# Kernel optimization log

Hardware: AMD Instinct MI355X
Metric: run time of the kernel (lower is better)

## Reference

```python
import jax, jax.numpy as jnp
import numpy as np

B, N, SK, D, H = 4, 1024, 1024, 1024, 16
HD = D // H  # head_dim = 64


def _ln(x, w, b):
    # torch LayerNorm: biased variance, eps=1e-6
    m = x.mean(-1, keepdims=True)
    v = x.var(-1, keepdims=True)
    return (x - m) * jax.lax.rsqrt(v + 1e-6) * w + b


def setup_inputs() -> dict:
    key = jax.random.key(0)
    ks = jax.random.split(key, 16)
    def w(k, shape, s=0.02):
        return jax.random.normal(k, shape, jnp.float32) * s
    return dict(
        x=jax.random.normal(ks[0], (B, N, D), jnp.float32),
        k=jax.random.normal(ks[1], (N, H, SK, HD), jnp.float32),
        v=jax.random.normal(ks[2], (N, H, SK, HD), jnp.float32),
        qkv_w=w(ks[3], (D, 3 * D)), qkv_b=w(ks[4], (3 * D,)),
        sa_proj_w=w(ks[5], (D, D)), sa_proj_b=w(ks[6], (D,)),
        q_w=w(ks[7], (D, D)), q_b=w(ks[8], (D,)),
        ed_proj_w=w(ks[9], (D, D)), ed_proj_b=w(ks[10], (D,)),
        fc1_w=w(ks[11], (D, 4 * D)), fc1_b=w(ks[12], (4 * D,)),
        fc2_w=w(ks[13], (4 * D, D)), fc2_b=w(ks[14], (D,)),
        ln1_w=jnp.ones((D,)), ln1_b=jnp.zeros((D,)),
        ln2_w=jnp.ones((D,)), ln2_b=jnp.zeros((D,)),
        ln3_w=jnp.ones((D,)), ln3_b=jnp.zeros((D,)),
    )


def reference(x, k, v, qkv_w, qkv_b, sa_proj_w, sa_proj_b, q_w, q_b,
              ed_proj_w, ed_proj_b, fc1_w, fc1_b, fc2_w, fc2_b,
              ln1_w, ln1_b, ln2_w, ln2_b, ln3_w, ln3_b):
    scale = HD ** -0.5
    # ---- SelfAttention (faithful to the original, unusual einsums) ----
    qkv = (x @ qkv_w + qkv_b).reshape(B, N, 3, H, HD).transpose(2, 1, 3, 0, 4)
    q_s, k_s, v_s = qkv[0], qkv[1], qkv[2]  # each [N, H, B, HD]
    # no shared contraction index between k and q -> outer product of reductions
    dp = jnp.einsum('kabc,qdef->qabe', k_s, q_s) * scale  # [N, H, B, B]
    sc = jax.nn.softmax(dp, axis=-1)  # attn_p = 0.0 -> dropout is identity
    wa = jnp.einsum('qabc,kdef->bqaf', sc, v_s).reshape(B, N, D)
    sa = wa @ sa_proj_w + sa_proj_b
    h1 = _ln(sa + x, ln1_w, ln1_b)
    # ---- EncoderDecoderAttention ----
    qc = (h1 @ q_w + q_b).reshape(B, N, H, HD).transpose(1, 2, 0, 3)  # [N, H, B, HD]
    dp2 = jnp.einsum('abkd,abqd->abqk', k, qc) * scale  # [N, H, B, SK]
    sc2 = jax.nn.softmax(dp2, axis=-1)
    wa2 = jnp.einsum('abts,abse->tabe', sc2, v).reshape(B, N, D)
    ca = wa2 @ ed_proj_w + ed_proj_b
    h2 = _ln(ca + x, ln2_w, ln2_b)  # residual uses x (as in source)
    # ---- MLP (exact GELU, p=0 dropout) ----
    z = jax.nn.gelu(h2 @ fc1_w + fc1_b, approximate=False) @ fc2_w + fc2_b
    return _ln(z + h2, ln3_w, ln3_b)
```

## Files before the change

### kernel.cpp

```cpp
#include <hip/hip_runtime.h>
#include <hip/hip_bf16.h>
#include <math.h>

typedef __attribute__((ext_vector_type(8))) short bf16x8;
typedef __attribute__((ext_vector_type(4))) float f32x4;

__device__ __forceinline__ void gll16(const void* g, const void* l) {
  __builtin_amdgcn_global_load_lds((__attribute__((address_space(1))) void*)g,
                                   (__attribute__((address_space(3))) void*)l, 16, 0, 0);
}

__device__ __forceinline__ unsigned short bf16bits(float f) {
  __hip_bfloat16 h = __float2bfloat16(f);
  return *reinterpret_cast<unsigned short*>(&h);
}

__global__ __launch_bounds__(256) void k_transpose4(
    const float* __restrict__ W0, __hip_bfloat16* __restrict__ T0,
    const float* __restrict__ W1, __hip_bfloat16* __restrict__ T1,
    const float* __restrict__ W2, __hip_bfloat16* __restrict__ T2,
    const float* __restrict__ W3, __hip_bfloat16* __restrict__ T3)
{
  __shared__ float t[32][33];
  int b = blockIdx.x;
  const float* W; __hip_bfloat16* T; int R, C, bx, by;
  if (b < 1024)      { W = W0; T = T0; R = 1024; C = 1024; bx = b & 31;  by = b >> 5; }
  else if (b < 2048) { b -= 1024; W = W1; T = T1; R = 1024; C = 1024; bx = b & 31;  by = b >> 5; }
  else if (b < 6144) { b -= 2048; W = W2; T = T2; R = 1024; C = 4096; bx = b & 127; by = b >> 7; }
  else               { b -= 6144; W = W3; T = T3; R = 4096; C = 1024; bx = b & 31;  by = b >> 5; }
  const int c0 = bx << 5, r0 = by << 5;
  const int tx = threadIdx.x & 31, ty = threadIdx.x >> 5;
#pragma unroll
  for (int i = 0; i < 32; i += 8)
    t[ty + i][tx] = W[(size_t)(r0 + ty + i) * C + c0 + tx];
  __syncthreads();
#pragma unroll
  for (int i = 0; i < 32; i += 8)
    T[(size_t)(c0 + ty + i) * R + r0 + tx] = __float2bfloat16(t[tx][ty + i]);
}

__global__ __launch_bounds__(256) void k_colsum_part(const float* __restrict__ x, float* __restrict__ part) {
  const int d = blockIdx.x * 256 + threadIdx.x;
  const int r0 = blockIdx.y * 128;
  float acc = 0.f;
  for (int r = 0; r < 128; ++r) acc += x[(size_t)(r0 + r) * 1024 + d];
  part[blockIdx.y * 1024 + d] = acc;
}

__global__ __launch_bounds__(256) void k_matvec_t(const float* __restrict__ part,
                                                  const float* __restrict__ qkv_w,
                                                  float* __restrict__ tmpt) {
  __shared__ float xs[1024];
  __shared__ float red[8][32];
#pragma unroll
  for (int jj = 0; jj < 4; ++jj) {
    const int d = threadIdx.x + (jj << 8);
    float a = 0.f;
    for (int y = 0; y < 32; ++y) a += part[y * 1024 + d];
    xs[d] = a;
  }
  __syncthreads();
  const int j = blockIdx.x * 32 + (threadIdx.x & 31);
  const int rg = threadIdx.x >> 5;
  float acc = 0.f;
  for (int r = rg; r < 1024; r += 8)
    acc += xs[r] * qkv_w[(size_t)r * 3072 + 2048 + j];
  red[rg][threadIdx.x & 31] = acc;
  __syncthreads();
  if (threadIdx.x < 32) {
    float s = 0.f;
    for (int gq = 0; gq < 8; ++gq) s += red[gq][threadIdx.x];
    tmpt[blockIdx.x * 32 + threadIdx.x] = s;
  }
}

__global__ __launch_bounds__(256) void k_matvec_sa(const float* __restrict__ tmpt,
                                                   const float* __restrict__ qkv_b,
                                                   const float* __restrict__ saw,
                                                   const float* __restrict__ sab,
                                                   float* __restrict__ sarow) {
  __shared__ float vs[64];
  __shared__ float red[8][32];
  if (threadIdx.x < 64) {
    float a = 0.f;
    for (int h = 0; h < 16; ++h)
      a += tmpt[h * 64 + threadIdx.x] + 4096.0f * qkv_b[2048 + h * 64 + threadIdx.x];
    vs[threadIdx.x] = a;
  }
  __syncthreads();
  const int j = blockIdx.x * 32 + (threadIdx.x & 31);
  const int rg = threadIdx.x >> 5;
  float acc = 0.f;
  for (int r = rg; r < 1024; r += 8)
    acc += vs[r & 63] * saw[(size_t)r * 1024 + j];
  red[rg][threadIdx.x & 31] = acc;
  __syncthreads();
  if (threadIdx.x < 32) {
    float s = 0.f;
    for (int gq = 0; gq < 8; ++gq) s += red[gq][threadIdx.x];
    sarow[blockIdx.x * 32 + threadIdx.x] = s + sab[blockIdx.x * 32 + threadIdx.x];
  }
}

__global__ __launch_bounds__(256) void k_ln(
    const float* __restrict__ a, const float* __restrict__ b, const float* __restrict__ c,
    const float* __restrict__ rowadd, const float* __restrict__ w,
    const float* __restrict__ bias, float* __restrict__ outF,
    __hip_bfloat16* __restrict__ outB)
{
  const size_t base = (size_t)blockIdx.x * 1024;
  const int d4 = threadIdx.x << 2;
  float4 t = *(const float4*)(a + base + d4);
  if (b) { const float4 u = *(const float4*)(b + base + d4);
           t.x += u.x; t.y += u.y; t.z += u.z; t.w += u.w; }
  if (c) { const float4 u = *(const float4*)(c + base + d4);
           t.x += u.x; t.y += u.y; t.z += u.z; t.w += u.w; }
  if (rowadd) { const float4 u = *(const float4*)(rowadd + d4);
                t.x += u.x; t.y += u.y; t.z += u.z; t.w += u.w; }
  float s1 = t.x + t.y + t.z + t.w;
  float s2 = t.x * t.x + t.y * t.y + t.z * t.z + t.w * t.w;
#pragma unroll
  for (int o = 32; o; o >>= 1) { s1 += __shfl_xor(s1, o); s2 += __shfl_xor(s2, o); }
  __shared__ float r1[4], r2[4];
  const int wv = threadIdx.x >> 6;
  if ((threadIdx.x & 63) == 0) { r1[wv] = s1; r2[wv] = s2; }
  __syncthreads();
  s1 = r1[0] + r1[1] + r1[2] + r1[3];
  s2 = r2[0] + r2[1] + r2[2] + r2[3];
  const float mean = s1 * (1.0f / 1024.0f);
  const float var = s2 * (1.0f / 1024.0f) - mean * mean;
  const float inv = rsqrtf(var + 1e-6f);
  const float4 w4 = *(const float4*)(w + d4);
  const float4 b4 = *(const float4*)(bias + d4);
  const float y0 = (t.x - mean) * inv * w4.x + b4.x;
  const float y1 = (t.y - mean) * inv * w4.y + b4.y;
  const float y2 = (t.z - mean) * inv * w4.z + b4.z;
  const float y3 = (t.w - mean) * inv * w4.w + b4.w;
  if (outF) *(float4*)(outF + base + d4) = make_float4(y0, y1, y2, y3);
  if (outB) {
    ushort4 u4; u4.x = bf16bits(y0); u4.y = bf16bits(y1); u4.z = bf16bits(y2); u4.w = bf16bits(y3);
    *(ushort4*)(outB + base + d4) = u4;
  }
}

template<int GELU, int OUTBF>
__global__ __launch_bounds__(256) void k_gemm_bt(
    const __hip_bfloat16* __restrict__ A, const __hip_bfloat16* __restrict__ BT,
    const float* __restrict__ bias, float* __restrict__ outF, float* __restrict__ outF2,
    __hip_bfloat16* __restrict__ outB, int M, int N, int K)
{
  __shared__ __align__(16) __hip_bfloat16 As[128 * 32];
  __shared__ __align__(16) __hip_bfloat16 Bs[128 * 32];
  const int tid = threadIdx.x;
  const int wave = tid >> 6, lane = tid & 63;
  const int m0 = blockIdx.y << 7, n0 = blockIdx.x << 7;
  const int kl = K / gridDim.z;
  const int ks = blockIdx.z * kl;
  float* outP = blockIdx.z ? outF2 : outF;
  const bool doBias = (blockIdx.z == 0);
  const int wr = wave >> 1, wc = wave & 1;
  const int fr = lane & 15, fq = lane >> 4;
  f32x4 acc[4][4] = {};
  const int srow = (lane >> 2);
  const int scol = (lane & 3) * 8;
  for (int k0 = ks; k0 < ks + kl; k0 += 32) {
#pragma unroll
    for (int i = 0; i < 2; ++i) {
      const int chunk = wave * 2 + i;
      const int row = (chunk << 4) + srow;
      gll16(A + (size_t)(m0 + row) * K + k0 + scol, As + (chunk << 9));
      gll16(BT + (size_t)(n0 + row) * K + k0 + scol, Bs + (chunk << 9));
    }
    __syncthreads();
    bf16x8 af[4], bfr[4];
#pragma unroll
    for (int m = 0; m < 4; ++m)
      af[m] = *(const bf16x8*)(As + ((wr << 6) + (m << 4) + fr) * 32 + (fq << 3));
#pragma unroll
    for (int nn = 0; nn < 4; ++nn)
      bfr[nn] = *(const bf16x8*)(Bs + ((wc << 6) + (nn << 4) + fr) * 32 + (fq << 3));
#pragma unroll
    for (int m = 0; m < 4; ++m)
#pragma unroll
      for (int nn = 0; nn < 4; ++nn)
        acc[m][nn] = __builtin_amdgcn_mfma_f32_16x16x32_bf16(af[m], bfr[nn], acc[m][nn], 0, 0, 0);
    __syncthreads();
  }
#pragma unroll
  for (int m = 0; m < 4; ++m) {
#pragma unroll
    for (int nn = 0; nn < 4; ++nn) {
      const int col = n0 + (wc << 6) + (nn << 4) + fr;
      const float bv = doBias ? bias[col] : 0.f;
#pragma unroll
      for (int j = 0; j < 4; ++j) {
        const int row = m0 + (wr << 6) + (m << 4) + (fq << 2) + j;
        float vv = acc[m][nn][j] + bv;
        if (GELU) vv = 0.5f * vv * (1.0f + erff(vv * 0.70710678118654752f));
        if (OUTBF) outB[(size_t)row * N + col] = __float2bfloat16(vv);
        else       outP[(size_t)row * N + col] = vv;
      }
    }
  }
}

__global__ __launch_bounds__(256) void k_attn(
    const float* __restrict__ kk, const float* __restrict__ vvg,
    const float* __restrict__ qc1, const float* __restrict__ qc2,
    __hip_bfloat16* __restrict__ wa2b)
{
  __shared__ __align__(16) float tile[2][32 * 64];
  __shared__ float p[4 * 1024];
  __shared__ __align__(16) float ql[4 * 64];
  const int tid = threadIdx.x;
  const int wave = tid >> 6, lane = tid & 63;
  const int n = blockIdx.x >> 4, h = blockIdx.x & 15;
  const size_t kvbase = (size_t)(n * 16 + h) * (1024 * 64);

  {
    const size_t qidx = ((size_t)wave * 1024 + n) * 1024 + h * 64 + lane;
    ql[tid] = (qc1[qidx] + qc2[qidx]) * 0.125f;
  }
  const float* qrow = ql + wave * 64;

  auto STAGE = [&](const float* __restrict__ src, int bi, int s0) {
#pragma unroll
    for (int i = 0; i < 2; ++i) {
      const int chunk = (wave << 1) + i;
      const int rl = (chunk << 2) + (lane >> 4);
      const int slot = (lane & 15) ^ (rl & 15);
      gll16(src + kvbase + (size_t)(s0 + rl) * 64 + (slot << 2), tile[bi] + (chunk << 8));
    }
  };

  STAGE(kk, 0, 0);
  __syncthreads();

  const int sl = lane & 31;
  const int dbase = (lane >> 5) << 3;
  const int sxx = sl & 15;
  for (int t = 0; t < 32; ++t) {
    if (t < 31) STAGE(kk, (t + 1) & 1, (t + 1) << 5);
    else        STAGE(vvg, 0, 0);
    const float* tl = tile[t & 1];
    float a = 0.f;
#pragma unroll
    for (int j = 0; j < 8; ++j) {
      const int c = dbase + j;
      const float4 kv = *(const float4*)(tl + sl * 64 + ((c ^ sxx) << 2));
      const float4 qa = *(const float4*)(qrow + (c << 2));
      a += kv.x * qa.x + kv.y * qa.y + kv.z * qa.z + kv.w * qa.w;
    }
    a += __shfl_xor(a, 32);
    if (lane < 32) p[(wave << 10) + (t << 5) + sl] = a;
    __syncthreads();
  }

  float mx = -1e30f;
#pragma unroll
  for (int j = 0; j < 16; ++j) mx = fmaxf(mx, p[(wave << 10) + (j << 6) + lane]);
#pragma unroll
  for (int o = 32; o; o >>= 1) mx = fmaxf(mx, __shfl_xor(mx, o));
  float sum = 0.f;
#pragma unroll
  for (int j = 0; j < 16; ++j) {
    const float e = __expf(p[(wave << 10) + (j << 6) + lane] - mx);
    p[(wave << 10) + (j << 6) + lane] = e;
    sum += e;
  }
#pragma unroll
  for (int o = 32; o; o >>= 1) sum += __shfl_xor(sum, o);
  const float inv = 1.0f / sum;

  const int sg = lane >> 4, e4 = lane & 15;
  float4 acc4 = make_float4(0.f, 0.f, 0.f, 0.f);
  for (int t = 0; t < 32; ++t) {
    if (t < 31) STAGE(vvg, (t + 1) & 1, (t + 1) << 5);
    const float* tl = tile[t & 1];
    const float* prow = p + (wave << 10) + (t << 5);
#pragma unroll
    for (int so = 0; so < 8; ++so) {
      const int s = (so << 2) + sg;
      const float pw = prow[s];
      const float4 vv = *(const float4*)(tl + s * 64 + ((e4 ^ (s & 15)) << 2));
      acc4.x += pw * vv.x; acc4.y += pw * vv.y; acc4.z += pw * vv.z; acc4.w += pw * vv.w;
    }
    __syncthreads();
  }
#pragma unroll
  for (int o = 16; o <= 32; o <<= 1) {
    acc4.x += __shfl_xor(acc4.x, o); acc4.y += __shfl_xor(acc4.y, o);
    acc4.z += __shfl_xor(acc4.z, o); acc4.w += __shfl_xor(acc4.w, o);
  }
  if (sg == 0) {
    ushort4 u4;
    u4.x = bf16bits(acc4.x * inv); u4.y = bf16bits(acc4.y * inv);
    u4.z = bf16bits(acc4.z * inv); u4.w = bf16bits(acc4.w * inv);
    *(ushort4*)(wa2b + ((size_t)wave * 1024 + n) * 1024 + h * 64 + (e4 << 2)) = u4;
  }
}

extern "C" void kernel_launch(void* const* d_in, const int* in_sizes, int n_in,
                              void* d_out, int out_size, void* d_ws, size_t ws_size,
                              hipStream_t stream)
{
  (void)in_sizes; (void)n_in; (void)out_size; (void)ws_size;
  const float* x     = (const float*)d_in[0];
  const float* kin   = (const float*)d_in[1];
  const float* vin   = (const float*)d_in[2];
  const float* qkv_w = (const float*)d_in[3];
  const float* qkv_b = (const float*)d_in[4];
  const float* sa_w  = (const float*)d_in[5];
  const float* sa_b  = (const float*)d_in[6];
  const float* q_w   = (const float*)d_in[7];
  const float* q_b   = (const float*)d_in[8];
  const float* ed_w  = (const float*)d_in[9];
  const float* ed_b  = (const float*)d_in[10];
  const float* fc1_w = (const float*)d_in[11];
  const float* fc1_b = (const float*)d_in[12];
  const float* fc2_w = (const float*)d_in[13];
  const float* fc2_b = (const float*)d_in[14];
  const float* ln1_w = (const float*)d_in[15];
  const float* ln1_b = (const float*)d_in[16];
  const float* ln2_w = (const float*)d_in[17];
  const float* ln2_b = (const float*)d_in[18];
  const float* ln3_w = (const float*)d_in[19];
  const float* ln3_b = (const float*)d_in[20];
  float* out = (float*)d_out;

  char* ws = (char*)d_ws;
  constexpr size_t MB = 1024ull * 1024ull;
  float* part  = (float*)(ws + 0);
  float* tmpt  = (float*)(ws + 192 * 1024);
  float* sarow = (float*)(ws + 256 * 1024);
  float* bufA  = (float*)(ws + 1 * MB);
  float* bufB  = (float*)(ws + 17 * MB);
  __hip_bfloat16* h1b  = (__hip_bfloat16*)(ws + 33 * MB);
  float*          h2   = (float*)(ws + 41 * MB);
  __hip_bfloat16* h2b  = (__hip_bfloat16*)(ws + 57 * MB);
  __hip_bfloat16* g    = (__hip_bfloat16*)(ws + 65 * MB);
  __hip_bfloat16* qwT  = (__hip_bfloat16*)(ws + 97 * MB);
  __hip_bfloat16* edwT = (__hip_bfloat16*)(ws + 99 * MB);
  __hip_bfloat16* f1wT = (__hip_bfloat16*)(ws + 101 * MB);
  __hip_bfloat16* f2wT = (__hip_bfloat16*)(ws + 109 * MB);
  __hip_bfloat16* wa2b = h1b;

  k_transpose4<<<dim3(10240), 256, 0, stream>>>(q_w, qwT, ed_w, edwT, fc1_w, f1wT, fc2_w, f2wT);
  k_colsum_part<<<dim3(4, 32), 256, 0, stream>>>(x, part);
  k_matvec_t<<<dim3(32), 256, 0, stream>>>(part, qkv_w, tmpt);
  k_matvec_sa<<<dim3(32), 256, 0, stream>>>(tmpt, qkv_b, sa_w, sa_b, sarow);
  k_ln<<<dim3(4096), 256, 0, stream>>>(x, nullptr, nullptr, sarow, ln1_w, ln1_b, nullptr, h1b);
  k_gemm_bt<0, 0><<<dim3(8, 32, 2), 256, 0, stream>>>(h1b, qwT, q_b, bufA, bufB, nullptr, 4096, 1024, 1024);
  k_attn<<<dim3(16384), 256, 0, stream>>>(kin, vin, bufA, bufB, wa2b);
  k_gemm_bt<0, 0><<<dim3(8, 32, 2), 256, 0, stream>>>(wa2b, edwT, ed_b, bufA, bufB, nullptr, 4096, 1024, 1024);
  k_ln<<<dim3(4096), 256, 0, stream>>>(bufA, bufB, x, nullptr, ln2_w, ln2_b, h2, h2b);
  k_gemm_bt<1, 1><<<dim3(32, 32), 256, 0, stream>>>(h2b, f1wT, fc1_b, nullptr, nullptr, g, 4096, 4096, 1024);
  k_gemm_bt<0, 0><<<dim3(8, 32, 2), 256, 0, stream>>>(g, f2wT, fc2_b, bufA, bufB, nullptr, 4096, 1024, 4096);
  k_ln<<<dim3(4096), 256, 0, stream>>>(bufA, bufB, h2, nullptr, ln3_w, ln3_b, out, nullptr);
}
```

Measured before the change: 1.769 ms.

## Deepen K/V staging to 4-buffer ring with explicit vmcnt waits in attention

Replaces the double-buffered K then V loops in the cross-attention kernel with a single 64-step loop over a 4-slot LDS ring. It keeps three tile loads in flight and uses explicit s_waitcnt vmcnt plus a raw barrier instead of __syncthreads. The goal is to hide global-to-LDS latency of the memory-bound K/V streaming, including across the K-to-V transition. LDS use grows to 4 tiles, which may reduce occupancy, and correctness now depends on the hand-written vmcnt counts.

```diff
diff --git a/kernel.cpp b/kernel.cpp
--- a/kernel.cpp
+++ b/kernel.cpp
@@ -209,7 +209,7 @@
     const float* __restrict__ qc1, const float* __restrict__ qc2,
     __hip_bfloat16* __restrict__ wa2b)
 {
-  __shared__ __align__(16) float tile[2][32 * 64];
+  __shared__ __align__(16) float tile[4][32 * 64];
   __shared__ float p[4 * 1024];
   __shared__ __align__(16) float ql[4 * 64];
   const int tid = threadIdx.x;
@@ -223,69 +223,72 @@
   }
   const float* qrow = ql + wave * 64;
 
-  auto STAGE = [&](const float* __restrict__ src, int bi, int s0) {
+  auto STAGE = [&](int u) {
+    const float* __restrict__ src = (u < 32) ? kk : vvg;
+    const int s0 = (u & 31) << 5;
 #pragma unroll
     for (int i = 0; i < 2; ++i) {
       const int chunk = (wave << 1) + i;
       const int rl = (chunk << 2) + (lane >> 4);
       const int slot = (lane & 15) ^ (rl & 15);
-      gll16(src + kvbase + (size_t)(s0 + rl) * 64 + (slot << 2), tile[bi] + (chunk << 8));
+      gll16(src + kvbase + (size_t)(s0 + rl) * 64 + (slot << 2), tile[u & 3] + (chunk << 8));
     }
   };
 
-  STAGE(kk, 0, 0);
-  __syncthreads();
+  STAGE(0); STAGE(1); STAGE(2);
 
   const int sl = lane & 31;
   const int dbase = (lane >> 5) << 3;
   const int sxx = sl & 15;
-  for (int t = 0; t < 32; ++t) {
-    if (t < 31) STAGE(kk, (t + 1) & 1, (t + 1) << 5);
-    else        STAGE(vvg, 0, 0);
-    const float* tl = tile[t & 1];
-    float a = 0.f;
-#pragma unroll
-    for (int j = 0; j < 8; ++j) {
-      const int c = dbase + j;
-      const float4 kv = *(const float4*)(tl + sl * 64 + ((c ^ sxx) << 2));
-      const float4 qa = *(const float4*)(qrow + (c << 2));
-      a += kv.x * qa.x + kv.y * qa.y + kv.z * qa.z + kv.w * qa.w;
-    }
-    a += __shfl_xor(a, 32);
-    if (lane < 32) p[(wave << 10) + (t << 5) + sl] = a;
-    __syncthreads();
-  }
-
-  float mx = -1e30f;
-#pragma unroll
-  for (int j = 0; j < 16; ++j) mx = fmaxf(mx, p[(wave << 10) + (j << 6) + lane]);
-#pragma unroll
-  for (int o = 32; o; o >>= 1) mx = fmaxf(mx, __shfl_xor(mx, o));
-  float sum = 0.f;
-#pragma unroll
-  for (int j = 0; j < 16; ++j) {
-    const float e = __expf(p[(wave << 10) + (j << 6) + lane] - mx);
-    p[(wave << 10) + (j << 6) + lane] = e;
-    sum += e;
-  }
-#pragma unroll
-  for (int o = 32; o; o >>= 1) sum += __shfl_xor(sum, o);
-  const float inv = 1.0f / sum;
-
   const int sg = lane >> 4, e4 = lane & 15;
   float4 acc4 = make_float4(0.f, 0.f, 0.f, 0.f);
-  for (int t = 0; t < 32; ++t) {
-    if (t < 31) STAGE(vvg, (t + 1) & 1, (t + 1) << 5);
-    const float* tl = tile[t & 1];
-    const float* prow = p + (wave << 10) + (t << 5);
-#pragma unroll
-    for (int so = 0; so < 8; ++so) {
-      const int s = (so << 2) + sg;
-      const float pw = prow[s];
-      const float4 vv = *(const float4*)(tl + s * 64 + ((e4 ^ (s & 15)) << 2));
-      acc4.x += pw * vv.x; acc4.y += pw * vv.y; acc4.z += pw * vv.z; acc4.w += pw * vv.w;
+  float inv = 0.f;
+
+  for (int u = 0; u < 64; ++u) {
+    if (u < 62)       asm volatile("s_waitcnt vmcnt(4)" ::: "memory");
+    else if (u == 62) asm volatile("s_waitcnt vmcnt(2)" ::: "memory");
+    else              asm volatile("s_waitcnt vmcnt(0)" ::: "memory");
+    __builtin_amdgcn_s_barrier();
+    if (u < 61) STAGE(u + 3);
+    const float* tl = tile[u & 3];
+    if (u < 32) {
+      float a = 0.f;
+#pragma unroll
+      for (int j = 0; j < 8; ++j) {
+        const int c = dbase + j;
+        const float4 kv = *(const float4*)(tl + sl * 64 + ((c ^ sxx) << 2));
+        const float4 qa = *(const float4*)(qrow + (c << 2));
+        a += kv.x * qa.x + kv.y * qa.y + kv.z * qa.z + kv.w * qa.w;
+      }
+      a += __shfl_xor(a, 32);
+      if (lane < 32) p[(wave << 10) + (u << 5) + sl] = a;
+    } else {
+      if (u == 32) {
+        float mx = -1e30f;
+#pragma unroll
+        for (int j = 0; j < 16; ++j) mx = fmaxf(mx, p[(wave << 10) + (j << 6) + lane]);
+#pragma unroll
+        for (int o = 32; o; o >>= 1) mx = fmaxf(mx, __shfl_xor(mx, o));
+        float sum = 0.f;
+#pragma unroll
+        for (int j = 0; j < 16; ++j) {
+          const float e = __expf(p[(wave << 10) + (j << 6) + lane] - mx);
+          p[(wave << 10) + (j << 6) + lane] = e;
+          sum += e;
+        }
+#pragma unroll
+        for (int o = 32; o; o >>= 1) sum += __shfl_xor(sum, o);
+        inv = 1.0f / sum;
+      }
+      const float* prow = p + (wave << 10) + ((u - 32) << 5);
+#pragma unroll
+      for (int so = 0; so < 8; ++so) {
+        const int s = (so << 2) + sg;
+        const float pw = prow[s];
+        const float4 vv = *(const float4*)(tl + s * 64 + ((e4 ^ (s & 15)) << 2));
+        acc4.x += pw * vv.x; acc4.y += pw * vv.y; acc4.z += pw * vv.z; acc4.w += pw * vv.w;
+      }
     }
-    __syncthreads();
   }
 #pragma unroll
   for (int o = 16; o <= 32; o <<= 1) {
```

Measured after the change: 1.895 ms. +7.1%, slower.
